# Performance work log

Hardware: AMD Instinct MI355X
Metric: run time of the kernel (lower is better)

## Reference

```python
import jax, jax.numpy as jnp
import numpy as np

B, S, D = 8, 1024, 1024
H, KV, HD = 16, 16, 64
NDIM = 2
EPS = 1e-6


def rms_norm(x, weight=None, eps=EPS):
    var = jnp.mean(jnp.square(x), axis=-1, keepdims=True)
    out = x * jax.lax.rsqrt(var + eps)
    if weight is not None:
        out = out * weight
    return out


def rotate_half(x):
    half = x.shape[-1] // 2
    return jnp.concatenate((-x[..., half:], x[..., :half]), axis=-1)


def multidim_rope(x, cos, sin, ndim):
    # x: [B,S,H,HD]; cos,sin: [B,S,HD]; head_dim split into ndim contiguous
    # chunks of size per = 2*(HD // (2*ndim)); rotate-half applied per chunk.
    b, s, h, hd = x.shape
    per = 2 * (hd // (2 * ndim))
    xg = x.reshape(b, s, h, ndim, per)
    cg = cos.reshape(b, s, 1, ndim, per)
    sg = sin.reshape(b, s, 1, ndim, per)
    out = xg * cg + rotate_half(xg) * sg
    return out.reshape(b, s, h, hd)


def setup_inputs() -> dict:
    key = jax.random.key(0)
    ks = jax.random.split(key, 10)
    scale = 1.0 / np.sqrt(D)
    return {
        "hidden_states": jax.random.normal(ks[0], (B, S, D), jnp.float32),
        "cos": jax.random.uniform(ks[1], (B, S, HD), jnp.float32, -1.0, 1.0),
        "sin": jax.random.uniform(ks[2], (B, S, HD), jnp.float32, -1.0, 1.0),
        "position_ids": jax.random.randint(ks[3], (B, S, NDIM), 0, 32, jnp.int32),
        "wq": jax.random.normal(ks[4], (D, H * HD), jnp.float32) * scale,
        "wk": jax.random.normal(ks[5], (D, KV * HD), jnp.float32) * scale,
        "wv": jax.random.normal(ks[6], (D, KV * HD), jnp.float32) * scale,
        "wo": jax.random.normal(ks[7], (H * HD, D), jnp.float32) * scale,
        "q_norm_w": jnp.ones((HD,), jnp.float32),
        "k_norm_w": jnp.ones((HD,), jnp.float32),
    }


def reference(hidden_states, cos, sin, position_ids, wq, wk, wv, wo, q_norm_w, k_norm_w):
    b, s, _ = hidden_states.shape
    ndim = position_ids.shape[-1]

    q = (hidden_states @ wq).reshape(b, s, H, HD)
    q = rms_norm(q, q_norm_w)
    q = multidim_rope(q, cos, sin, ndim)

    k = (hidden_states @ wk).reshape(b, s, KV, HD)
    k = rms_norm(k, k_norm_w)
    k = multidim_rope(k, cos, sin, ndim)

    v = (hidden_states @ wv).reshape(b, s, KV, HD)
    v = rms_norm(v, None)  # v_norm has no weight

    # Full (non-causal) vision attention, scaling = 1.0
    scores = jnp.einsum("bqhd,bkhd->bhqk", q, k)
    probs = jax.nn.softmax(scores, axis=-1)
    attn = jnp.einsum("bhqk,bkhd->bqhd", probs, v).reshape(b, s, H * HD)

    return attn @ wo
```

## Files before the change

kernel.cpp:

```cpp
#include <hip/hip_runtime.h>
#include <hip/hip_bf16.h>

typedef __attribute__((ext_vector_type(8))) short bf16x8;
typedef __attribute__((ext_vector_type(4))) short bf16x4;
typedef __attribute__((ext_vector_type(4))) float f32x4;

struct __align__(16) V16 { unsigned long long a, b; };

__device__ __forceinline__ float bf2f(unsigned short u) {
  union { unsigned int i; float f; } c; c.i = ((unsigned int)u) << 16; return c.f;
}
__device__ __forceinline__ unsigned short f2bf(float f) {
  unsigned int u; __builtin_memcpy(&u, &f, 4);
  u += 0x7FFFu + ((u >> 16) & 1u);
  return (unsigned short)(u >> 16);
}

__device__ __forceinline__ void async16(unsigned short* lds,
                                        const unsigned short* g) {
  __builtin_amdgcn_global_load_lds(
      (const __attribute__((address_space(1))) unsigned int*)g,
      (__attribute__((address_space(3))) unsigned int*)lds, 16, 0, 0);
}

__device__ __forceinline__ void xcd_swizzle(int& bx, int& by) {
  const int nx = (int)gridDim.x;
  const int nwg = nx * (int)gridDim.y;
  if ((nwg & 7) == 0) {
    int orig = by * nx + bx;
    int swz = (orig & 7) * (nwg >> 3) + (orig >> 3);
    bx = swz % nx;
    by = swz / nx;
  }
}

#define FP32_MAGIC 0x3F800000u

__device__ __forceinline__ void cvt_seg(
    const void* __restrict__ src, unsigned short* __restrict__ dst,
    int n4, int i, int stride, bool f32)
{
  if (f32) {
    const float* s = (const float*)src;
    for (; i < n4; i += stride) {
      float4 v = *(const float4*)(s + (size_t)i * 4);
      ushort4 o4 = { f2bf(v.x), f2bf(v.y), f2bf(v.z), f2bf(v.w) };
      *(ushort4*)(dst + (size_t)i * 4) = o4;
    }
  } else {
    const unsigned short* s = (const unsigned short*)src;
    for (; i < n4; i += stride)
      *(ushort4*)(dst + (size_t)i * 4) = *(const ushort4*)(s + (size_t)i * 4);
  }
}

__global__ __launch_bounds__(256) void cvt_bf16(
    const void* __restrict__ src, size_t srcOff,
    unsigned short* __restrict__ dst, int n4,
    const unsigned int* __restrict__ fmt)
{
  const bool f32 = (fmt[0] == FP32_MAGIC);
  const int i = blockIdx.x * blockDim.x + threadIdx.x;
  const int stride = gridDim.x * blockDim.x;
  const void* s = f32 ? (const void*)((const float*)src + srcOff)
                      : (const void*)((const unsigned short*)src + srcOff);
  cvt_seg(s, dst, n4, i, stride, f32);
}

__global__ __launch_bounds__(256) void prep_all(
    const void* __restrict__ wq, const void* __restrict__ wk,
    const void* __restrict__ wv, const void* __restrict__ wo,
    unsigned short* __restrict__ wqT, unsigned short* __restrict__ wkT,
    unsigned short* __restrict__ wvT, unsigned short* __restrict__ woT,
    const void* __restrict__ hid, const void* __restrict__ cosr,
    const void* __restrict__ sinr, const void* __restrict__ qnw,
    const void* __restrict__ knw,
    unsigned short* __restrict__ hb, unsigned short* __restrict__ csb,
    unsigned short* __restrict__ snb, unsigned short* __restrict__ qnb,
    unsigned short* __restrict__ knb,
    int hidden_n4, const unsigned int* __restrict__ fmt)
{
  __shared__ __align__(16) unsigned short T[64][72];
  const bool f32 = (fmt[0] == FP32_MAGIC);
  const int bx = blockIdx.x, tid = threadIdx.x;

  if (bx < 1024) {
    const int z = bx >> 8, tile = bx & 255;
    const void* src = (z == 0) ? wq : (z == 1) ? wk : (z == 2) ? wv : wo;
    unsigned short* dstT = (z == 0) ? wqT : (z == 1) ? wkT
                         : (z == 2) ? wvT : woT;
    const int k0 = (tile >> 4) * 64, n0 = (tile & 15) * 64;
    const int rl = tid >> 3, cl = (tid & 7) * 8;

#pragma unroll
    for (int p = 0; p < 2; ++p) {
      int r = rl + p * 32;
      int csl = cl ^ (r & 56);
      if (f32) {
        const float* s = (const float*)src + (size_t)(k0 + r) * 1024 + n0 + cl;
        float4 v0 = *(const float4*)s, v1 = *(const float4*)(s + 4);
        unsigned short* t = &T[r][csl];
        t[0]=f2bf(v0.x); t[1]=f2bf(v0.y); t[2]=f2bf(v0.z); t[3]=f2bf(v0.w);
        t[4]=f2bf(v1.x); t[5]=f2bf(v1.y); t[6]=f2bf(v1.z); t[7]=f2bf(v1.w);
      } else {
        *(V16*)&T[r][csl] = *(const V16*)((const unsigned short*)src +
                                          (size_t)(k0 + r) * 1024 + n0 + cl);
      }
    }
    __syncthreads();

#pragma unroll
    for (int p = 0; p < 2; ++p) {
      int u = tid + p * 256;
      int d = u >> 3, sc = (u & 7) * 8;
      unsigned short tmp[8];
#pragma unroll
      for (int i = 0; i < 8; ++i) tmp[i] = T[sc + i][d ^ sc];
      *(V16*)&dstT[(size_t)(n0 + d) * 1024 + k0 + sc] = *(V16*)tmp;
    }
    return;
  }

  const int cx = bx - 1024;
  if (cx < 2048) {
    if (hidden_n4 > 0)
      cvt_seg(hid, hb, hidden_n4, cx * 256 + tid, 2048 * 256, f32);
  } else if (cx < 2176) {
    cvt_seg(cosr, csb, 131072, (cx - 2048) * 256 + tid, 128 * 256, f32);
  } else if (cx < 2304) {
    cvt_seg(sinr, snb, 131072, (cx - 2176) * 256 + tid, 128 * 256, f32);
  } else {
    if (tid < 16)       cvt_seg(qnw, qnb, 16, tid, 16, f32);
    else if (tid < 32)  cvt_seg(knw, knb, 16, tid - 16, 16, f32);
  }
}

#define TK 64
#define GK 1024
#define QTM 256
#define QTN 128

__global__ __launch_bounds__(512, 2) void gemm_qkv(
    const unsigned short* __restrict__ A,
    const unsigned short* __restrict__ Bt,
    unsigned short* __restrict__ Cq,
    unsigned short* __restrict__ Ck,
    unsigned short* __restrict__ Cv,
    const unsigned short* __restrict__ cs,
    const unsigned short* __restrict__ sn,
    const unsigned short* __restrict__ qw,
    const unsigned short* __restrict__ kw,
    int M)
{
  __shared__ __align__(16) unsigned short LDSu[2 * (QTM + QTN) * TK];

  const int tid  = threadIdx.x;
  const int wave = tid >> 6;
  const int lane = tid & 63;
  const int quad = lane >> 4;
  const int l16  = lane & 15;
  const int wr   = wave >> 1;
  const int wc   = wave & 1;
  const int bm = blockIdx.x * QTM;
  const int bn = blockIdx.y * QTN;

  const f32x4 z = {0.f, 0.f, 0.f, 0.f};
  f32x4 acc[4][4];
#pragma unroll
  for (int i = 0; i < 4; ++i)
#pragma unroll
    for (int j = 0; j < 4; ++j) acc[i][j] = z;

  const int lrow = lane >> 3;
  const int gcol = ((lane & 7) ^ lrow) * 8;
  const unsigned short* aP = A  + (size_t)(bm + wave * 8 + lrow) * GK + gcol;
  const unsigned short* bP = Bt + (size_t)(bn + wave * 8 + lrow) * GK + gcol;
  const int cswz = l16 & 7;

  unsigned short* As0 = LDSu;
  unsigned short* Bs0 = LDSu + QTM * TK;
  const int BUFS = (QTM + QTN) * TK;

  auto STAGE_A = [&](int b, int t, int p) {
    async16(As0 + b * BUFS + (p * 64 + wave * 8) * TK,
            aP + (size_t)(p * 64) * GK + t * TK);
  };
  auto STAGE_B = [&](int b, int t, int p) {
    async16(Bs0 + b * BUFS + (p * 64 + wave * 8) * TK,
            bP + (size_t)(p * 64) * GK + t * TK);
  };

  STAGE_A(0, 0, 0); STAGE_A(0, 0, 1); STAGE_A(0, 0, 2); STAGE_A(0, 0, 3);
  STAGE_B(0, 0, 0); STAGE_B(0, 0, 1);

#pragma unroll 2
  for (int t = 0; t < 16; ++t) {
    const int cur = t & 1, nxt = cur ^ 1;

    if (t < 15) {
      STAGE_A(nxt, t + 1, 0); STAGE_A(nxt, t + 1, 1); STAGE_B(nxt, t + 1, 0);
      asm volatile("s_waitcnt vmcnt(3)" ::: "memory");
    } else {
      asm volatile("s_waitcnt vmcnt(0)" ::: "memory");
    }
    asm volatile("s_barrier" ::: "memory");

    const unsigned short* Ab = As0 + cur * BUFS;
    const unsigned short* Bb = Bs0 + cur * BUFS;
    bf16x8 af[4][2], bfv[4][2];
#pragma unroll
    for (int ks = 0; ks < 2; ++ks) {
      const int pc = ((ks * 4 + quad) ^ cswz) * 8;
#pragma unroll
      for (int mt = 0; mt < 4; ++mt)
        af[mt][ks] = *(const bf16x8*)&Ab[(wr * 64 + mt * 16 + l16) * TK + pc];
#pragma unroll
      for (int nt = 0; nt < 4; ++nt)
        bfv[nt][ks] = *(const bf16x8*)&Bb[(wc * 64 + nt * 16 + l16) * TK + pc];
    }

    __builtin_amdgcn_s_setprio(1);
#pragma unroll
    for (int mt = 0; mt < 4; ++mt)
#pragma unroll
      for (int nt = 0; nt < 4; ++nt)
        acc[mt][nt] = __builtin_amdgcn_mfma_f32_16x16x32_bf16(
            af[mt][0], bfv[nt][0], acc[mt][nt], 0, 0, 0);
    __builtin_amdgcn_s_setprio(0);
    asm volatile("s_barrier" ::: "memory");

    if (t < 15) {
      STAGE_A(nxt, t + 1, 2); STAGE_A(nxt, t + 1, 3); STAGE_B(nxt, t + 1, 1);
    }
    __builtin_amdgcn_s_setprio(1);
#pragma unroll
    for (int mt = 0; mt < 4; ++mt)
#pragma unroll
      for (int nt = 0; nt < 4; ++nt)
        acc[mt][nt] = __builtin_amdgcn_mfma_f32_16x16x32_bf16(
            af[mt][1], bfv[nt][1], acc[mt][nt], 0, 0, 0);
    __builtin_amdgcn_s_setprio(0);
    asm volatile("s_barrier" ::: "memory");
  }

  const int which = bn >> 10;
  const int colbase = (bn & 1023) + wc * 64;

  if (which == 2) {
    unsigned short* Tw = LDSu + wave * 4096;
#pragma unroll
    for (int mt = 0; mt < 4; ++mt)
#pragma unroll
      for (int r = 0; r < 4; ++r) {
        const int s = mt * 16 + quad * 4 + r;
        float x0 = acc[mt][0][r], x1 = acc[mt][1][r];
        float x2 = acc[mt][2][r], x3 = acc[mt][3][r];
        float ss = x0 * x0 + x1 * x1 + x2 * x2 + x3 * x3;
        ss += __shfl_xor(ss, 1);
        ss += __shfl_xor(ss, 2);
        ss += __shfl_xor(ss, 4);
        ss += __shfl_xor(ss, 8);
        const float inv = rsqrtf(ss * (1.f / 64.f) + 1e-6f);
        const int sw = (s >> 3) << 3;
#pragma unroll
        for (int nt = 0; nt < 4; ++nt)
          Tw[s * 64 + ((nt * 16 + l16) ^ sw)] = f2bf(acc[mt][nt][r] * inv);
      }
    __builtin_amdgcn_wave_barrier();

    const int vhead = ((bm >> 10) * 16 + (colbase >> 6)) * 64;
    const int sbase = (bm & 1023) + wr * 64;
    const int c  = lane & 7;
    const int sg = c * 8;
    const int dl = lane >> 3;
    const int m0 = 2 * c, m1 = 2 * c + 1;
    const int P0 = 32 * (m0 >> 3) + 8 * (m0 & 3) + 4 * ((m0 >> 2) & 1);
    const int P1 = 32 * (m1 >> 3) + 8 * (m1 & 3) + 4 * ((m1 >> 2) & 1);
#pragma unroll
    for (int p = 0; p < 8; ++p) {
      const int d = p * 8 + dl;
      union { unsigned short u[8]; unsigned long long q[2]; } tmp;
#pragma unroll
      for (int i = 0; i < 8; ++i)
        tmp.u[i] = Tw[(sg + i) * 64 + (d ^ sg)];
      unsigned short* dst = &Cv[(size_t)(vhead + d) * 1024 + sbase];
      *(unsigned long long*)(dst + P0) = tmp.q[0];
      *(unsigned long long*)(dst + P1) = tmp.q[1];
    }
    return;
  }

  unsigned short* Cd = (which == 0) ? Cq : Ck;
  float wgt[4];
#pragma unroll
  for (int nt = 0; nt < 4; ++nt) {
    int d = nt * 16 + l16;
    wgt[nt] = (which == 0) ? bf2f(qw[d]) * 1.44269504f : bf2f(kw[d]);
  }

#pragma unroll
  for (int mt = 0; mt < 4; ++mt)
#pragma unroll
    for (int r = 0; r < 4; ++r) {
      const int row = bm + wr * 64 + mt * 16 + quad * 4 + r;
      float x0 = acc[mt][0][r], x1 = acc[mt][1][r];
      float x2 = acc[mt][2][r], x3 = acc[mt][3][r];
      float ss = x0 * x0 + x1 * x1 + x2 * x2 + x3 * x3;
      ss += __shfl_xor(ss, 1);
      ss += __shfl_xor(ss, 2);
      ss += __shfl_xor(ss, 4);
      ss += __shfl_xor(ss, 8);
      const float inv = rsqrtf(ss * (1.f / 64.f) + 1e-6f);
      float y[4] = { x0 * inv * wgt[0], x1 * inv * wgt[1],
                     x2 * inv * wgt[2], x3 * inv * wgt[3] };
      const unsigned short* cp = cs + (size_t)row * 64 + l16;
      const unsigned short* sp = sn + (size_t)row * 64 + l16;
#pragma unroll
      for (int nt = 0; nt < 4; ++nt) {
        float c = bf2f(cp[nt * 16]), s = bf2f(sp[nt * 16]);
        float part = (nt & 1) ? y[nt ^ 1] : -y[nt ^ 1];
        Cd[(size_t)row * 1024 + colbase + nt * 16 + l16] =
            f2bf(y[nt] * c + part * s);
      }
    }
}

__global__ __launch_bounds__(512, 2) void gemm_bf16(
    const unsigned short* __restrict__ A,
    const unsigned short* __restrict__ Bt,
    void* __restrict__ C, size_t cOff,
    const unsigned int* __restrict__ outFmt,
    int M, int N)
{
  __shared__ __align__(16) unsigned short LDSu[2 * (QTM + QTN) * TK];

  const int tid  = threadIdx.x;
  const int wave = tid >> 6;
  const int lane = tid & 63;
  const int quad = lane >> 4;
  const int l16  = lane & 15;
  const int wr   = wave >> 1;
  const int wc   = wave & 1;
  const int bm = blockIdx.x * QTM;
  const int bn = blockIdx.y * QTN;

  const f32x4 z = {0.f, 0.f, 0.f, 0.f};
  f32x4 acc[4][4];
#pragma unroll
  for (int i = 0; i < 4; ++i)
#pragma unroll
    for (int j = 0; j < 4; ++j) acc[i][j] = z;

  const int lrow = lane >> 3;
  const int gcol = ((lane & 7) ^ lrow) * 8;
  const unsigned short* aP = A  + (size_t)(bm + wave * 8 + lrow) * GK + gcol;
  const unsigned short* bP = Bt + (size_t)(bn + wave * 8 + lrow) * GK + gcol;
  const int cswz = l16 & 7;

  unsigned short* As0 = LDSu;
  unsigned short* Bs0 = LDSu + QTM * TK;
  const int BUFS = (QTM + QTN) * TK;

  auto STAGE_A = [&](int b, int t, int p) {
    async16(As0 + b * BUFS + (p * 64 + wave * 8) * TK,
            aP + (size_t)(p * 64) * GK + t * TK);
  };
  auto STAGE_B = [&](int b, int t, int p) {
    async16(Bs0 + b * BUFS + (p * 64 + wave * 8) * TK,
            bP + (size_t)(p * 64) * GK + t * TK);
  };

  STAGE_A(0, 0, 0); STAGE_A(0, 0, 1); STAGE_A(0, 0, 2); STAGE_A(0, 0, 3);
  STAGE_B(0, 0, 0); STAGE_B(0, 0, 1);

#pragma unroll 2
  for (int t = 0; t < 16; ++t) {
    const int cur = t & 1, nxt = cur ^ 1;

    if (t < 15) {
      STAGE_A(nxt, t + 1, 0); STAGE_A(nxt, t + 1, 1); STAGE_B(nxt, t + 1, 0);
      asm volatile("s_waitcnt vmcnt(3)" ::: "memory");
    } else {
      asm volatile("s_waitcnt vmcnt(0)" ::: "memory");
    }
    asm volatile("s_barrier" ::: "memory");

    const unsigned short* Ab = As0 + cur * BUFS;
    const unsigned short* Bb = Bs0 + cur * BUFS;
    bf16x8 af[4][2], bfv[4][2];
#pragma unroll
    for (int ks = 0; ks < 2; ++ks) {
      const int pc = ((ks * 4 + quad) ^ cswz) * 8;
#pragma unroll
      for (int mt = 0; mt < 4; ++mt)
        af[mt][ks] = *(const bf16x8*)&Ab[(wr * 64 + mt * 16 + l16) * TK + pc];
#pragma unroll
      for (int nt = 0; nt < 4; ++nt)
        bfv[nt][ks] = *(const bf16x8*)&Bb[(wc * 64 + nt * 16 + l16) * TK + pc];
    }

    __builtin_amdgcn_s_setprio(1);
#pragma unroll
    for (int mt = 0; mt < 4; ++mt)
#pragma unroll
      for (int nt = 0; nt < 4; ++nt)
        acc[mt][nt] = __builtin_amdgcn_mfma_f32_16x16x32_bf16(
            af[mt][0], bfv[nt][0], acc[mt][nt], 0, 0, 0);
    __builtin_amdgcn_s_setprio(0);
    asm volatile("s_barrier" ::: "memory");

    if (t < 15) {
      STAGE_A(nxt, t + 1, 2); STAGE_A(nxt, t + 1, 3); STAGE_B(nxt, t + 1, 1);
    }
    __builtin_amdgcn_s_setprio(1);
#pragma unroll
    for (int mt = 0; mt < 4; ++mt)
#pragma unroll
      for (int nt = 0; nt < 4; ++nt)
        acc[mt][nt] = __builtin_amdgcn_mfma_f32_16x16x32_bf16(
            af[mt][1], bfv[nt][1], acc[mt][nt], 0, 0, 0);
    __builtin_amdgcn_s_setprio(0);
    asm volatile("s_barrier" ::: "memory");
  }

  const bool of32 = (outFmt != nullptr) && (outFmt[0] == FP32_MAGIC);
  float* Cf = (float*)C + cOff;
  unsigned short* Ch = (unsigned short*)C + cOff;

#pragma unroll
  for (int mt = 0; mt < 4; ++mt)
#pragma unroll
    for (int nt = 0; nt < 4; ++nt)
#pragma unroll
      for (int r = 0; r < 4; ++r) {
        int row = bm + wr * 64 + mt * 16 + quad * 4 + r;
        int col = bn + wc * 64 + nt * 16 + l16;
        size_t idx = (size_t)row * N + col;
        if (of32) Cf[idx] = acc[mt][nt][r];
        else      Ch[idx] = f2bf(acc[mt][nt][r]);
      }
}

__global__ __launch_bounds__(256, 3) void attn_fused(
    const unsigned short* __restrict__ q,
    const unsigned short* __restrict__ k,
    const unsigned short* __restrict__ vt,
    unsigned short* __restrict__ o)
{
  __shared__ __align__(16) unsigned short Ks[2][64][64];
  __shared__ __align__(16) unsigned short Vs[2][64][64];

  int bxs = blockIdx.x, bys = blockIdx.y;
  xcd_swizzle(bxs, bys);

  const int tid  = threadIdx.x;
  const int wave = tid >> 6;
  const int lane = tid & 63;
  const int quad = lane >> 4;
  const int l16  = lane & 15;
  const int bh = bys;
  const int b  = bh >> 4, h = bh & 15;
  const int qbase = bxs * 128 + wave * 32;
  const size_t bbase = (size_t)b * 1024;

  bf16x8 qfA[2], qfB[2];
  {
    const unsigned short* qp = q + (bbase + qbase + l16) * 1024 + h * 64;
    qfA[0] = *(const bf16x8*)(qp + quad * 8);
    qfA[1] = *(const bf16x8*)(qp + 32 + quad * 8);
    qfB[0] = *(const bf16x8*)(qp + 16 * 1024 + quad * 8);
    qfB[1] = *(const bf16x8*)(qp + 16 * 1024 + 32 + quad * 8);
  }

  const f32x4 z = {0.f, 0.f, 0.f, 0.f};
  f32x4 ofA[5], ofB[5];
#pragma unroll
  for (int nt = 0; nt < 5; ++nt) { ofA[nt] = z; ofB[nt] = z; }
  float mA = -1e30f, mB = -1e30f;

  const bf16x8 onesv = { 0x3F80, 0x3F80, 0x3F80, 0x3F80,
                         0x3F80, 0x3F80, 0x3F80, 0x3F80 };

  const int lrow = lane >> 3;
  const int gcol = ((lane & 7) ^ lrow) * 8;
  const unsigned short* kP = k  + (bbase + wave * 8 + lrow) * 1024 + h * 64 + gcol;
  const unsigned short* vP = vt + ((size_t)bh * 64 + wave * 8 + lrow) * 1024 + gcol;
  const int cswz = l16 & 7;

  auto STAGE = [&](int buf, int kt) {
#pragma unroll
    for (int p = 0; p < 2; ++p) {
      async16(&Ks[buf][p * 32 + wave * 8][0], kP + ((size_t)kt * 64 + p * 32) * 1024);
      async16(&Vs[buf][p * 32 + wave * 8][0], vP + (size_t)p * 32 * 1024 + kt * 64);
    }
  };

  STAGE(0, 0);
  __syncthreads();

#pragma unroll 2
  for (int kt = 0; kt < 16; ++kt) {
    const int cur = kt & 1;
    if (kt < 15) STAGE(cur ^ 1, kt + 1);

    f32x4 sA[4], sB[4];
#pragma unroll
    for (int nt = 0; nt < 4; ++nt) { sA[nt] = z; sB[nt] = z; }
    __builtin_amdgcn_s_setprio(1);
#pragma unroll
    for (int s = 0; s < 2; ++s) {
      const int pc = ((s * 4 + quad) ^ cswz) * 8;
#pragma unroll
      for (int nt = 0; nt < 4; ++nt) {
        bf16x8 kf = *(const bf16x8*)&Ks[cur][nt * 16 + l16][pc];
        sA[nt] = __builtin_amdgcn_mfma_f32_16x16x32_bf16(kf, qfA[s], sA[nt], 0, 0, 0);
        sB[nt] = __builtin_amdgcn_mfma_f32_16x16x32_bf16(kf, qfB[s], sB[nt], 0, 0, 0);
      }
    }
    __builtin_amdgcn_s_setprio(0);

    float mxA, mxB;
    {
      float a0 = fmaxf(fmaxf(sA[0][0], sA[0][1]), fmaxf(sA[0][2], sA[0][3]));
      float a1 = fmaxf(fmaxf(sA[1][0], sA[1][1]), fmaxf(sA[1][2], sA[1][3]));
      float a2 = fmaxf(fmaxf(sA[2][0], sA[2][1]), fmaxf(sA[2][2], sA[2][3]));
      float a3 = fmaxf(fmaxf(sA[3][0], sA[3][1]), fmaxf(sA[3][2], sA[3][3]));
      mxA = fmaxf(fmaxf(a0, a1), fmaxf(a2, a3));
      mxA = fmaxf(mxA, __shfl_xor(mxA, 16));
      mxA = fmaxf(mxA, __shfl_xor(mxA, 32));
      float b0 = fmaxf(fmaxf(sB[0][0], sB[0][1]), fmaxf(sB[0][2], sB[0][3]));
      float b1 = fmaxf(fmaxf(sB[1][0], sB[1][1]), fmaxf(sB[1][2], sB[1][3]));
      float b2 = fmaxf(fmaxf(sB[2][0], sB[2][1]), fmaxf(sB[2][2], sB[2][3]));
      float b3 = fmaxf(fmaxf(sB[3][0], sB[3][1]), fmaxf(sB[3][2], sB[3][3]));
      mxB = fmaxf(fmaxf(b0, b1), fmaxf(b2, b3));
      mxB = fmaxf(mxB, __shfl_xor(mxB, 16));
      mxB = fmaxf(mxB, __shfl_xor(mxB, 32));
    }

    if (!__all((mxA - mA <= 11.5f) && (mxB - mB <= 11.5f))) {
      float mnA = fmaxf(mA, mxA);
      float mnB = fmaxf(mB, mxB);
      float aA = __builtin_amdgcn_exp2f(mA - mnA);
      float aB = __builtin_amdgcn_exp2f(mB - mnB);
      mA = mnA; mB = mnB;
      float arA[4], arB[4];
#pragma unroll
      for (int r = 0; r < 4; ++r) {
        arA[r] = __shfl(aA, quad * 4 + r);
        arB[r] = __shfl(aB, quad * 4 + r);
      }
#pragma unroll
      for (int nt = 0; nt < 5; ++nt)
#pragma unroll
        for (int r = 0; r < 4; ++r) {
          ofA[nt][r] *= arA[r];
          ofB[nt][r] *= arB[r];
        }
    }

    bf16x8 pA[2], pB[2];
#pragma unroll
    for (int nt = 0; nt < 4; ++nt)
#pragma unroll
      for (int r = 0; r < 4; ++r) {
        pA[nt >> 1][(nt & 1) * 4 + r] =
            (short)f2bf(__builtin_amdgcn_exp2f(sA[nt][r] - mA));
        pB[nt >> 1][(nt & 1) * 4 + r] =
            (short)f2bf(__builtin_amdgcn_exp2f(sB[nt][r] - mB));
      }

    __builtin_amdgcn_s_setprio(1);
#pragma unroll
    for (int s = 0; s < 2; ++s) {
      const int pc = ((s * 4 + quad) ^ cswz) * 8;
#pragma unroll
      for (int nt = 0; nt < 4; ++nt) {
        bf16x8 vf = *(const bf16x8*)&Vs[cur][nt * 16 + l16][pc];
        ofA[nt] = __builtin_amdgcn_mfma_f32_16x16x32_bf16(pA[s], vf, ofA[nt], 0, 0, 0);
        ofB[nt] = __builtin_amdgcn_mfma_f32_16x16x32_bf16(pB[s], vf, ofB[nt], 0, 0, 0);
      }
      ofA[4] = __builtin_amdgcn_mfma_f32_16x16x32_bf16(pA[s], onesv, ofA[4], 0, 0, 0);
      ofB[4] = __builtin_amdgcn_mfma_f32_16x16x32_bf16(pB[s], onesv, ofB[4], 0, 0, 0);
    }
    __builtin_amdgcn_s_setprio(0);

    __syncthreads();
  }

  float ilA[4], ilB[4];
#pragma unroll
  for (int r = 0; r < 4; ++r) {
    ilA[r] = 1.f / ofA[4][r];
    ilB[r] = 1.f / ofB[4][r];
  }
#pragma unroll
  for (int nt = 0; nt < 4; ++nt)
#pragma unroll
    for (int r = 0; r < 4; ++r) {
      int row = qbase + quad * 4 + r;
      o[(bbase + row) * 1024 + h * 64 + nt * 16 + l16] = f2bf(ofA[nt][r] * ilA[r]);
      o[(bbase + row + 16) * 1024 + h * 64 + nt * 16 + l16] = f2bf(ofB[nt][r] * ilB[r]);
    }
}

extern "C" void kernel_launch(void* const* d_in, const int* in_sizes, int n_in,
                              void* d_out, int out_size, void* d_ws, size_t ws_size,
                              hipStream_t stream) {
  const void* hidden = d_in[0];
  const void* cosr   = d_in[1];
  const void* sinr   = d_in[2];
  const void* wq     = d_in[4];
  const void* wk     = d_in[5];
  const void* wv     = d_in[6];
  const void* wo     = d_in[7];
  const void* qnw    = d_in[8];
  const void* knw    = d_in[9];
  const unsigned int* fmt = (const unsigned int*)qnw;

  const size_t MEG = 1024 * 1024;
  dim3 blk(256);
  dim3 blk512(512);
  unsigned short* w = (unsigned short*)d_ws;

  if (ws_size >= (size_t)60 * MEG) {
    unsigned short* hb   = w;
    unsigned short* wqT  = w + 8 * MEG;
    unsigned short* wkT  = w + 9 * MEG;
    unsigned short* wvT  = w + 10 * MEG;
    unsigned short* woT  = w + 11 * MEG;
    unsigned short* csb  = w + 12 * MEG;
    unsigned short* snb  = w + 12 * MEG + 512 * 1024;
    unsigned short* qnb  = w + 13 * MEG;
    unsigned short* knb  = w + 13 * MEG + 64;
    unsigned short* qb   = w + 14 * MEG;
    unsigned short* kb   = w + 22 * MEG;
    unsigned short* vtb  = (unsigned short*)d_out;
    unsigned short* ab   = qb;

    prep_all<<<dim3(3329), blk, 0, stream>>>(wq, wk, wv, wo,
                                             wqT, wkT, wvT, woT,
                                             hidden, cosr, sinr, qnw, knw,
                                             hb, csb, snb, qnb, knb,
                                             2 * (int)MEG, fmt);

    const int M = 8192;
    gemm_qkv<<<dim3(M / QTM, 24), blk512, 0, stream>>>(hb, wqT, qb, kb, vtb,
                                                       csb, snb, qnb, knb, M);
    attn_fused<<<dim3(8, 8 * 16), blk, 0, stream>>>(qb, kb, vtb, ab);
    gemm_bf16<<<dim3(M / QTM, 8), blk512, 0, stream>>>(ab, woT, d_out, 0, fmt,
                                                       M, 1024);
  } else {
    unsigned short* wqT  = w;
    unsigned short* wkT  = w + 1 * MEG;
    unsigned short* wvT  = w + 2 * MEG;
    unsigned short* woT  = w + 3 * MEG;
    unsigned short* csb  = w + 4 * MEG;
    unsigned short* snb  = w + 4 * MEG + 512 * 1024;
    unsigned short* qnb  = w + 5 * MEG;
    unsigned short* knb  = w + 5 * MEG + 64;
    unsigned short* hbb  = w + 6 * MEG;
    unsigned short* qb   = w + 7 * MEG;
    unsigned short* kb   = w + 8 * MEG;
    unsigned short* vtb  = w + 10 * MEG;

    prep_all<<<dim3(3329), blk, 0, stream>>>(wq, wk, wv, wo,
                                             wqT, wkT, wvT, woT,
                                             hidden, cosr, sinr, qnw, knw,
                                             nullptr, csb, snb, qnb, knb,
                                             0, fmt);

    const int Mb = 1024;
    for (int b = 0; b < 8; ++b) {
      cvt_bf16<<<dim3(512), blk, 0, stream>>>(hidden, (size_t)b * MEG, hbb,
                                              (int)(MEG / 4), fmt);
      gemm_qkv<<<dim3(Mb / QTM, 24), blk512, 0, stream>>>(
          hbb, wqT, qb, kb, vtb, csb + (size_t)b * 64 * 1024,
          snb + (size_t)b * 64 * 1024, qnb, knb, Mb);
      attn_fused<<<dim3(8, 16), blk, 0, stream>>>(qb, kb, vtb, qb);
      gemm_bf16<<<dim3(Mb / QTM, 8), blk512, 0, stream>>>(qb, woT, d_out,
                                                          (size_t)b * MEG, fmt,
                                                          Mb, 1024);
    }
  }
}
```

Measured before the change: 245.5 us.

## Process 64 query rows per wave in attention to double K/V reuse

Each wave in the fused attention kernel now handles four 16-row query groups instead of two, so a workgroup covers 256 query rows and the grid's x dimension halves. Each K/V tile staged in LDS is reused across twice as many query rows, which halves the global/LDS traffic for K and V per unit of work. The cost is much higher register pressure (more accumulators and score tiles), so occupancy drops to 2 waves per SIMD target and the loop unroll is removed. There are also fewer workgroups to fill the GPU (512 blocks).

After: 245.2 us. Within noise of the previous version (-0.2%).

```diff
diff --git a/kernel.cpp b/kernel.cpp
--- a/kernel.cpp
+++ b/kernel.cpp
@@ -441,7 +441,7 @@
       }
 }
 
-__global__ __launch_bounds__(256, 3) void attn_fused(
+__global__ __launch_bounds__(256, 2) void attn_fused(
     const unsigned short* __restrict__ q,
     const unsigned short* __restrict__ k,
     const unsigned short* __restrict__ vt,
@@ -460,23 +460,26 @@
   const int l16  = lane & 15;
   const int bh = bys;
   const int b  = bh >> 4, h = bh & 15;
-  const int qbase = bxs * 128 + wave * 32;
+  const int qbase = bxs * 256 + wave * 64;
   const size_t bbase = (size_t)b * 1024;
 
-  bf16x8 qfA[2], qfB[2];
+  bf16x8 qf[4][2];
   {
     const unsigned short* qp = q + (bbase + qbase + l16) * 1024 + h * 64;
-    qfA[0] = *(const bf16x8*)(qp + quad * 8);
-    qfA[1] = *(const bf16x8*)(qp + 32 + quad * 8);
-    qfB[0] = *(const bf16x8*)(qp + 16 * 1024 + quad * 8);
-    qfB[1] = *(const bf16x8*)(qp + 16 * 1024 + 32 + quad * 8);
+#pragma unroll
+    for (int hh = 0; hh < 4; ++hh) {
+      qf[hh][0] = *(const bf16x8*)(qp + hh * 16 * 1024 + quad * 8);
+      qf[hh][1] = *(const bf16x8*)(qp + hh * 16 * 1024 + 32 + quad * 8);
+    }
   }
 
   const f32x4 z = {0.f, 0.f, 0.f, 0.f};
-  f32x4 ofA[5], ofB[5];
-#pragma unroll
-  for (int nt = 0; nt < 5; ++nt) { ofA[nt] = z; ofB[nt] = z; }
-  float mA = -1e30f, mB = -1e30f;
+  f32x4 of[4][5];
+#pragma unroll
+  for (int hh = 0; hh < 4; ++hh)
+#pragma unroll
+    for (int nt = 0; nt < 5; ++nt) of[hh][nt] = z;
+  float m[4] = { -1e30f, -1e30f, -1e30f, -1e30f };
 
   const bf16x8 onesv = { 0x3F80, 0x3F80, 0x3F80, 0x3F80,
                          0x3F80, 0x3F80, 0x3F80, 0x3F80 };
@@ -498,14 +501,15 @@
   STAGE(0, 0);
   __syncthreads();
 
-#pragma unroll 2
   for (int kt = 0; kt < 16; ++kt) {
     const int cur = kt & 1;
     if (kt < 15) STAGE(cur ^ 1, kt + 1);
 
-    f32x4 sA[4], sB[4];
-#pragma unroll
-    for (int nt = 0; nt < 4; ++nt) { sA[nt] = z; sB[nt] = z; }
+    f32x4 sf[4][4];
+#pragma unroll
+    for (int hh = 0; hh < 4; ++hh)
+#pragma unroll
+      for (int nt = 0; nt < 4; ++nt) sf[hh][nt] = z;
     __builtin_amdgcn_s_setprio(1);
 #pragma unroll
     for (int s = 0; s < 2; ++s) {
@@ -513,61 +517,58 @@
 #pragma unroll
       for (int nt = 0; nt < 4; ++nt) {
         bf16x8 kf = *(const bf16x8*)&Ks[cur][nt * 16 + l16][pc];
-        sA[nt] = __builtin_amdgcn_mfma_f32_16x16x32_bf16(kf, qfA[s], sA[nt], 0, 0, 0);
-        sB[nt] = __builtin_amdgcn_mfma_f32_16x16x32_bf16(kf, qfB[s], sB[nt], 0, 0, 0);
+#pragma unroll
+        for (int hh = 0; hh < 4; ++hh)
+          sf[hh][nt] = __builtin_amdgcn_mfma_f32_16x16x32_bf16(
+              kf, qf[hh][s], sf[hh][nt], 0, 0, 0);
       }
     }
     __builtin_amdgcn_s_setprio(0);
 
-    float mxA, mxB;
-    {
-      float a0 = fmaxf(fmaxf(sA[0][0], sA[0][1]), fmaxf(sA[0][2], sA[0][3]));
-      float a1 = fmaxf(fmaxf(sA[1][0], sA[1][1]), fmaxf(sA[1][2], sA[1][3]));
-      float a2 = fmaxf(fmaxf(sA[2][0], sA[2][1]), fmaxf(sA[2][2], sA[2][3]));
-      float a3 = fmaxf(fmaxf(sA[3][0], sA[3][1]), fmaxf(sA[3][2], sA[3][3]));
-      mxA = fmaxf(fmaxf(a0, a1), fmaxf(a2, a3));
-      mxA = fmaxf(mxA, __shfl_xor(mxA, 16));
-      mxA = fmaxf(mxA, __shfl_xor(mxA, 32));
-      float b0 = fmaxf(fmaxf(sB[0][0], sB[0][1]), fmaxf(sB[0][2], sB[0][3]));
-      float b1 = fmaxf(fmaxf(sB[1][0], sB[1][1]), fmaxf(sB[1][2], sB[1][3]));
-      float b2 = fmaxf(fmaxf(sB[2][0], sB[2][1]), fmaxf(sB[2][2], sB[2][3]));
-      float b3 = fmaxf(fmaxf(sB[3][0], sB[3][1]), fmaxf(sB[3][2], sB[3][3]));
-      mxB = fmaxf(fmaxf(b0, b1), fmaxf(b2, b3));
-      mxB = fmaxf(mxB, __shfl_xor(mxB, 16));
-      mxB = fmaxf(mxB, __shfl_xor(mxB, 32));
-    }
-
-    if (!__all((mxA - mA <= 11.5f) && (mxB - mB <= 11.5f))) {
-      float mnA = fmaxf(mA, mxA);
-      float mnB = fmaxf(mB, mxB);
-      float aA = __builtin_amdgcn_exp2f(mA - mnA);
-      float aB = __builtin_amdgcn_exp2f(mB - mnB);
-      mA = mnA; mB = mnB;
-      float arA[4], arB[4];
-#pragma unroll
-      for (int r = 0; r < 4; ++r) {
-        arA[r] = __shfl(aA, quad * 4 + r);
-        arB[r] = __shfl(aB, quad * 4 + r);
-      }
-#pragma unroll
-      for (int nt = 0; nt < 5; ++nt)
-#pragma unroll
-        for (int r = 0; r < 4; ++r) {
-          ofA[nt][r] *= arA[r];
-          ofB[nt][r] *= arB[r];
-        }
-    }
-
-    bf16x8 pA[2], pB[2];
-#pragma unroll
-    for (int nt = 0; nt < 4; ++nt)
-#pragma unroll
-      for (int r = 0; r < 4; ++r) {
-        pA[nt >> 1][(nt & 1) * 4 + r] =
-            (short)f2bf(__builtin_amdgcn_exp2f(sA[nt][r] - mA));
-        pB[nt >> 1][(nt & 1) * 4 + r] =
-            (short)f2bf(__builtin_amdgcn_exp2f(sB[nt][r] - mB));
-      }
+    float mx[4];
+#pragma unroll
+    for (int hh = 0; hh < 4; ++hh) {
+      float a0 = fmaxf(fmaxf(sf[hh][0][0], sf[hh][0][1]),
+                       fmaxf(sf[hh][0][2], sf[hh][0][3]));
+      float a1 = fmaxf(fmaxf(sf[hh][1][0], sf[hh][1][1]),
+                       fmaxf(sf[hh][1][2], sf[hh][1][3]));
+      float a2 = fmaxf(fmaxf(sf[hh][2][0], sf[hh][2][1]),
+                       fmaxf(sf[hh][2][2], sf[hh][2][3]));
+      float a3 = fmaxf(fmaxf(sf[hh][3][0], sf[hh][3][1]),
+                       fmaxf(sf[hh][3][2], sf[hh][3][3]));
+      float v = fmaxf(fmaxf(a0, a1), fmaxf(a2, a3));
+      v = fmaxf(v, __shfl_xor(v, 16));
+      v = fmaxf(v, __shfl_xor(v, 32));
+      mx[hh] = v;
+    }
+
+    bool ok = (mx[0] - m[0] <= 11.5f) && (mx[1] - m[1] <= 11.5f) &&
+              (mx[2] - m[2] <= 11.5f) && (mx[3] - m[3] <= 11.5f);
+    if (!__all(ok)) {
+#pragma unroll
+      for (int hh = 0; hh < 4; ++hh) {
+        float mn = fmaxf(m[hh], mx[hh]);
+        float al = __builtin_amdgcn_exp2f(m[hh] - mn);
+        m[hh] = mn;
+        float ar[4];
+#pragma unroll
+        for (int r = 0; r < 4; ++r) ar[r] = __shfl(al, quad * 4 + r);
+#pragma unroll
+        for (int nt = 0; nt < 5; ++nt)
+#pragma unroll
+          for (int r = 0; r < 4; ++r) of[hh][nt][r] *= ar[r];
+      }
+    }
+
+    bf16x8 pf[4][2];
+#pragma unroll
+    for (int hh = 0; hh < 4; ++hh)
+#pragma unroll
+      for (int nt = 0; nt < 4; ++nt)
+#pragma unroll
+        for (int r = 0; r < 4; ++r)
+          pf[hh][nt >> 1][(nt & 1) * 4 + r] =
+              (short)f2bf(__builtin_amdgcn_exp2f(sf[hh][nt][r] - m[hh]));
 
     __builtin_amdgcn_s_setprio(1);
 #pragma unroll
@@ -576,31 +577,35 @@
 #pragma unroll
       for (int nt = 0; nt < 4; ++nt) {
         bf16x8 vf = *(const bf16x8*)&Vs[cur][nt * 16 + l16][pc];
-        ofA[nt] = __builtin_amdgcn_mfma_f32_16x16x32_bf16(pA[s], vf, ofA[nt], 0, 0, 0);
-        ofB[nt] = __builtin_amdgcn_mfma_f32_16x16x32_bf16(pB[s], vf, ofB[nt], 0, 0, 0);
-      }
-      ofA[4] = __builtin_amdgcn_mfma_f32_16x16x32_bf16(pA[s], onesv, ofA[4], 0, 0, 0);
-      ofB[4] = __builtin_amdgcn_mfma_f32_16x16x32_bf16(pB[s], onesv, ofB[4], 0, 0, 0);
+#pragma unroll
+        for (int hh = 0; hh < 4; ++hh)
+          of[hh][nt] = __builtin_amdgcn_mfma_f32_16x16x32_bf16(
+              pf[hh][s], vf, of[hh][nt], 0, 0, 0);
+      }
+#pragma unroll
+      for (int hh = 0; hh < 4; ++hh)
+        of[hh][4] = __builtin_amdgcn_mfma_f32_16x16x32_bf16(
+            pf[hh][s], onesv, of[hh][4], 0, 0, 0);
     }
     __builtin_amdgcn_s_setprio(0);
 
     __syncthreads();
   }
 
-  float ilA[4], ilB[4];
-#pragma unroll
-  for (int r = 0; r < 4; ++r) {
-    ilA[r] = 1.f / ofA[4][r];
-    ilB[r] = 1.f / ofB[4][r];
-  }
-#pragma unroll
-  for (int nt = 0; nt < 4; ++nt)
-#pragma unroll
-    for (int r = 0; r < 4; ++r) {
-      int row = qbase + quad * 4 + r;
-      o[(bbase + row) * 1024 + h * 64 + nt * 16 + l16] = f2bf(ofA[nt][r] * ilA[r]);
-      o[(bbase + row + 16) * 1024 + h * 64 + nt * 16 + l16] = f2bf(ofB[nt][r] * ilB[r]);
-    }
+#pragma unroll
+  for (int hh = 0; hh < 4; ++hh) {
+    float il[4];
+#pragma unroll
+    for (int r = 0; r < 4; ++r) il[r] = 1.f / of[hh][4][r];
+#pragma unroll
+    for (int nt = 0; nt < 4; ++nt)
+#pragma unroll
+      for (int r = 0; r < 4; ++r) {
+        int row = qbase + hh * 16 + quad * 4 + r;
+        o[(bbase + row) * 1024 + h * 64 + nt * 16 + l16] =
+            f2bf(of[hh][nt][r] * il[r]);
+      }
+  }
 }
 
 extern "C" void kernel_launch(void* const* d_in, const int* in_sizes, int n_in,
@@ -646,7 +651,7 @@
     const int M = 8192;
     gemm_qkv<<<dim3(M / QTM, 24), blk512, 0, stream>>>(hb, wqT, qb, kb, vtb,
                                                        csb, snb, qnb, knb, M);
-    attn_fused<<<dim3(8, 8 * 16), blk, 0, stream>>>(qb, kb, vtb, ab);
+    attn_fused<<<dim3(4, 8 * 16), blk, 0, stream>>>(qb, kb, vtb, ab);
     gemm_bf16<<<dim3(M / QTM, 8), blk512, 0, stream>>>(ab, woT, d_out, 0, fmt,
                                                        M, 1024);
   } else {
@@ -676,7 +681,7 @@
       gemm_qkv<<<dim3(Mb / QTM, 24), blk512, 0, stream>>>(
           hbb, wqT, qb, kb, vtb, csb + (size_t)b * 64 * 1024,
           snb + (size_t)b * 64 * 1024, qnb, knb, Mb);
-      attn_fused<<<dim3(8, 16), blk, 0, stream>>>(qb, kb, vtb, qb);
+      attn_fused<<<dim3(4, 16), blk, 0, stream>>>(qb, kb, vtb, qb);
       gemm_bf16<<<dim3(Mb / QTM, 8), blk512, 0, stream>>>(qb, woT, d_out,
                                                           (size_t)b * MEG, fmt,
                                                           Mb, 1024);
```
